# Optimization experiments

Measured on AMD Instinct MI355X. Metric: run time of the kernel, lower is better.

Reference implementation:

```python
import jax, jax.numpy as jnp
import numpy as np

N = 1024      # num nodes
E = 16384     # num edges
P = 8192      # num query pairs
HD1 = 64      # hidden_dim_1
HD2 = 64      # hidden_dim_2
VOCAB = 1000  # max_x + 1
EPS = 1e-5


def gcn_conv(x, W, b, src, dst, n):
    # PyG GCNConv: h = D^{-1/2} (A + I) D^{-1/2} (x @ W) + b
    h = x @ W
    loop = jnp.arange(n)
    s = jnp.concatenate([src, loop])
    d = jnp.concatenate([dst, loop])
    deg = jnp.zeros((n,), h.dtype).at[d].add(1.0)
    dis = jax.lax.rsqrt(deg)  # deg >= 1 due to self-loops
    norm = dis[s] * dis[d]
    out = jnp.zeros_like(h).at[d].add(norm[:, None] * h[s])
    return out + b


def graph_norm(x, w, b, alpha):
    # PyG GraphNorm with a single graph: stats over node dim (axis 0)
    mean = jnp.mean(x, axis=0, keepdims=True)
    sh = x - alpha * mean
    var = jnp.mean(sh * sh, axis=0, keepdims=True)
    return w * sh / jnp.sqrt(var + EPS) + b


def _forward(x_ids, ei, pos, emb, gW0, gb0, gnw0, gnb0, gna0, gW1, gb1,
             gnw1, gnb1, gna1, m1W, m1b, m2W, m2b, m3W, m3b,
             gn3w, gn3b, gn3a, ldW, ldb):
    n = x_ids.shape[0]
    src, dst = ei[0], ei[1]
    x = emb[x_ids]                                            # [n, HD1]
    # 1-WL: two GCNConv -> GraphNorm -> ReLU blocks
    x = jax.nn.relu(graph_norm(gcn_conv(x, gW0, gb0, src, dst, n), gnw0, gnb0, gna0))
    x = jax.nn.relu(graph_norm(gcn_conv(x, gW1, gb1, src, dst, n), gnw1, gnb1, gna1))
    # O(n^2) outer product: X[i,j] = x[i] * x[j]
    X = x[:, None, :] * x[None, :, :]                         # [n, n, HD1]
    eim = jnp.zeros((n, n), x.dtype).at[src, dst].set(1.0)    # adjacency indicator
    # add_chan = eye(n) @ eim = eim
    X = jnp.concatenate([X, eim[:, :, None]], axis=-1)        # [n, n, HD1+1]
    # 2-FWL refinement (layer2 = 1)
    x1 = jax.nn.relu(X @ m1W + m1b)                           # [n, n, HD2]
    x2 = jax.nn.relu(X @ m2W + m2b)                           # [n, n, HD2]
    prod = jnp.einsum('ikc,kjc->ijc', x1, x2)                 # per-channel bmm
    X = jnp.concatenate([X, prod], axis=-1)                   # [n, n, HD1+1+HD2]
    X = jax.nn.relu(graph_norm(X @ m3W + m3b, gn3w, gn3b, gn3a))
    # symmetric mul-pool then gather query pairs
    X = X * jnp.transpose(X, (1, 0, 2))                       # [n, n, HD2]
    feat = X[pos[:, 0], pos[:, 1]]                            # [P, HD2]
    return feat @ ldW + ldb                                   # [P, 1]


def setup_inputs() -> dict:
    key = jax.random.key(0)
    ks = jax.random.split(key, 12)
    sc = lambda k, s: jax.random.normal(k, s, jnp.float32) * 0.05
    d = {}
    d['x_ids'] = jax.random.randint(ks[0], (N,), 0, VOCAB)
    d['ei'] = jax.random.randint(ks[1], (2, E), 0, N)
    d['pos'] = jax.random.randint(ks[2], (P, 2), 0, N)
    d['emb'] = sc(ks[3], (VOCAB, HD1))
    d['gW0'] = sc(ks[4], (HD1, HD1)); d['gb0'] = jnp.zeros((HD1,), jnp.float32)
    d['gnw0'] = jnp.ones((HD1,), jnp.float32); d['gnb0'] = jnp.zeros((HD1,), jnp.float32); d['gna0'] = jnp.ones((HD1,), jnp.float32)
    d['gW1'] = sc(ks[5], (HD1, HD1)); d['gb1'] = jnp.zeros((HD1,), jnp.float32)
    d['gnw1'] = jnp.ones((HD1,), jnp.float32); d['gnb1'] = jnp.zeros((HD1,), jnp.float32); d['gna1'] = jnp.ones((HD1,), jnp.float32)
    d['m1W'] = sc(ks[6], (HD1 + 1, HD2)); d['m1b'] = jnp.zeros((HD2,), jnp.float32)
    d['m2W'] = sc(ks[7], (HD1 + 1, HD2)); d['m2b'] = jnp.zeros((HD2,), jnp.float32)
    d['m3W'] = sc(ks[8], (HD2 + HD1 + 1, HD2)); d['m3b'] = jnp.zeros((HD2,), jnp.float32)
    d['gn3w'] = jnp.ones((HD2,), jnp.float32); d['gn3b'] = jnp.zeros((HD2,), jnp.float32); d['gn3a'] = jnp.ones((HD2,), jnp.float32)
    d['ldW'] = sc(ks[9], (HD2, 1)); d['ldb'] = jnp.zeros((1,), jnp.float32)
    return d


def reference(x_ids, ei, pos, emb, gW0, gb0, gnw0, gnb0, gna0, gW1, gb1,
              gnw1, gnb1, gna1, m1W, m1b, m2W, m2b, m3W, m3b,
              gn3w, gn3b, gn3a, ldW, ldb):
    return _forward(x_ids, ei, pos, emb, gW0, gb0, gnw0, gnb0, gna0, gW1, gb1,
                    gnw1, gnb1, gna1, m1W, m1b, m2W, m2b, m3W, m3b,
                    gn3w, gn3b, gn3a, ldW, ldb)
```

## Files before the change

### kernel.cpp

```cpp
#include <hip/hip_runtime.h>


typedef unsigned short u16;
typedef unsigned int u32;

#define DI static __device__ __forceinline__

DI float bf2f(u16 u) { union { u32 i; float f; } v; v.i = ((u32)u) << 16; return v.f; }
DI u16 f2bf(float f) {
  union { float f; u32 i; } v; v.f = f;
  u32 u = v.i;
  return (u16)((u + 0x7fffu + ((u >> 16) & 1u)) >> 16);
}

typedef __bf16 bf16x8 __attribute__((ext_vector_type(8)));
typedef float f32x4 __attribute__((ext_vector_type(4)));

#define MFMA16(a, b, c) __builtin_amdgcn_mfma_f32_16x16x32_bf16((a), (b), (c), 0, 0, 0)

typedef const __attribute__((address_space(1))) u32* gas1;
typedef __attribute__((address_space(3))) u32* las3;


__global__ void k_setup(const int* __restrict__ xids, const float* __restrict__ emb,
                        float* __restrict__ xf, float* __restrict__ deg,
                        u32* __restrict__ eimu) {
  int g = blockIdx.x * 256 + threadIdx.x;
  if (g < 262144) eimu[g] = 0u;
  if (g < 1024) deg[g] = 1.0f;
  if (g < 65536) {
    int i = g >> 6, d = g & 63;
    xf[g] = emb[xids[i] * 64 + d];
  }
}

__global__ void k_edges(const int* __restrict__ ei, float* __restrict__ deg,
                        unsigned char* __restrict__ eim) {
  int e = blockIdx.x * 256 + threadIdx.x;
  if (e < 16384) {
    int s = ei[e], d = ei[16384 + e];
    atomicAdd(&deg[d], 1.0f);
    eim[s * 1024 + d] = 1;
  }
}

__global__ void k_gemm_node(const float* __restrict__ xf, const float* __restrict__ W,
                            const float* __restrict__ gb, const float* __restrict__ deg,
                            float* __restrict__ h, float* __restrict__ agg) {
  __shared__ float xrow[64];
  int i = blockIdx.x, c = threadIdx.x;
  xrow[c] = xf[i * 64 + c];
  __syncthreads();
  float s = 0.f;
#pragma unroll
  for (int d = 0; d < 64; ++d) s += xrow[d] * W[d * 64 + c];
  h[i * 64 + c] = s;
  agg[i * 64 + c] = s / deg[i] + gb[c];
}

__global__ void k_agg(const int* __restrict__ ei, const float* __restrict__ deg,
                      const float* __restrict__ h, float* __restrict__ agg) {
  int g = blockIdx.x * 256 + threadIdx.x;
  int e = g >> 6, c = g & 63;
  int s = ei[e], d = ei[16384 + e];
  float nrm = rsqrtf(deg[s]) * rsqrtf(deg[d]);
  atomicAdd(&agg[d * 64 + c], nrm * h[s * 64 + c]);
}

__global__ void k_gnorm(const float* __restrict__ agg, const float* __restrict__ gw,
                        const float* __restrict__ gbb, const float* __restrict__ ga,
                        float* __restrict__ xf, u16* __restrict__ xb, int last) {
  int c = blockIdx.x, t = threadIdx.x;
  float s = 0.f, ss = 0.f;
  for (int i = t; i < 1024; i += 256) {
    float v = agg[i * 64 + c];
    s += v; ss += v * v;
  }
  __shared__ float Ls[256], Lss[256];
  Ls[t] = s; Lss[t] = ss;
  __syncthreads();
  for (int off = 128; off > 0; off >>= 1) {
    if (t < off) { Ls[t] += Ls[t + off]; Lss[t] += Lss[t + off]; }
    __syncthreads();
  }
  float m = Ls[0] * (1.f / 1024.f);
  float a = ga[c];
  float var = Lss[0] * (1.f / 1024.f) - (2.f * a - a * a) * m * m;
  float sc = gw[c] * rsqrtf(fmaxf(var, 0.f) + 1e-5f);
  float bb = gbb[c];
  for (int i = t; i < 1024; i += 256) {
    float v = agg[i * 64 + c];
    float y = fmaxf(sc * (v - a * m) + bb, 0.f);
    xf[i * 64 + c] = y;
    if (last) xb[i * 64 + c] = f2bf(y);
  }
}

__global__ __launch_bounds__(256, 2) void k_build12(
    const u16* __restrict__ xbg, const unsigned char* __restrict__ eim,
    const float* __restrict__ m1W, const float* __restrict__ m1b,
    const float* __restrict__ m2W, const float* __restrict__ m2b,
    u16* __restrict__ x1tg, u16* __restrict__ x2tg, int cbase) {
  __shared__ u16 As[128 * 80];
  __shared__ u16 Bs[128 * 80];
  __shared__ u16 Cs[64 * 140];
  __shared__ unsigned char El[128 * 132];
  __shared__ float wsc[64];
  int b = blockIdx.x;
  int cg = b & 3;
  int rest = b >> 2;
  int which = rest >> 6;
  int t6 = rest & 63;
  int rbase = (t6 >> 3) * 128, sbase = (t6 & 7) * 128;
  const float* W = which ? m2W : m1W;
  const float* bias = which ? m2b : m1b;
  u16* outg = which ? x2tg : x1tg;
  int t = threadIdx.x;
  {
    int row = t >> 1, half = t & 1;
    const u32* gB = (const u32*)(xbg + (sbase + row) * 64 + half * 32);
    u32* dstB = (u32*)&Bs[row * 80 + half * 32];
#pragma unroll
    for (int k = 0; k < 16; ++k) dstB[k] = gB[k];
    int ab = which ? sbase : rbase;
    int bb = which ? rbase : sbase;
    const u32* gE = (const u32*)(eim + (size_t)(ab + row) * 1024 + bb + half * 64);
    u32* dstE = (u32*)&El[row * 132 + half * 64];
#pragma unroll
    for (int k = 0; k < 16; ++k) dstE[k] = gE[k];
  }
  int lane = t & 63, w = t >> 6;
  int q = lane >> 4, r = lane & 15;
  int wr = w >> 1, wc = w & 1;
  for (int ci = 0; ci < 4; ++ci) {
    int cl = cg * 4 + ci;
    int c = cbase + cl;
    if (t < 64) wsc[t] = W[t * 64 + c];
    __syncthreads();
    {
      int row = t >> 1, half = t & 1;
      const u32* ga = (const u32*)(xbg + (rbase + row) * 64 + half * 32);
      u32* dstA = (u32*)&As[row * 80 + half * 32];
#pragma unroll
      for (int k = 0; k < 16; ++k) {
        u32 u = ga[k];
        float f0 = bf2f((u16)(u & 0xffffu)) * wsc[half * 32 + 2 * k];
        float f1 = bf2f((u16)(u >> 16)) * wsc[half * 32 + 2 * k + 1];
        dstA[k] = (u32)f2bf(f0) | ((u32)f2bf(f1) << 16);
      }
    }
    __syncthreads();
    f32x4 z4 = {0.f, 0.f, 0.f, 0.f};
    f32x4 acc[4][4];
#pragma unroll
    for (int mi = 0; mi < 4; ++mi)
#pragma unroll
      for (int ni = 0; ni < 4; ++ni) acc[mi][ni] = z4;
#pragma unroll
    for (int ks = 0; ks < 2; ++ks) {
      bf16x8 af[4], bfr[4];
#pragma unroll
      for (int mi = 0; mi < 4; ++mi)
        af[mi] = *(const bf16x8*)&As[(wr * 64 + mi * 16 + r) * 80 + ks * 32 + q * 8];
#pragma unroll
      for (int ni = 0; ni < 4; ++ni)
        bfr[ni] = *(const bf16x8*)&Bs[(wc * 64 + ni * 16 + r) * 80 + ks * 32 + q * 8];
#pragma unroll
      for (int mi = 0; mi < 4; ++mi)
#pragma unroll
        for (int ni = 0; ni < 4; ++ni) acc[mi][ni] = MFMA16(af[mi], bfr[ni], acc[mi][ni]);
    }
    float w64 = W[64 * 64 + c];
    float bsv = bias[c];
#pragma unroll
    for (int mi = 0; mi < 4; ++mi) {
#pragma unroll
      for (int ni = 0; ni < 4; ++ni) {
        int col = wc * 64 + ni * 16 + r;
#pragma unroll
        for (int tt = 0; tt < 4; ++tt) {
          int row2 = wr * 64 + mi * 16 + q * 4 + tt;
          float e = (float)(which ? El[col * 132 + row2] : El[row2 * 132 + col]);
          acc[mi][ni][tt] = fmaxf(acc[mi][ni][tt] + e * w64 + bsv, 0.f);
        }
      }
    }
    u16* outp = outg + (size_t)cl * 1048576;
#pragma unroll
    for (int p = 0; p < 2; ++p) {
      __syncthreads();
      if (wr == p) {
#pragma unroll
        for (int mi = 0; mi < 4; ++mi)
#pragma unroll
          for (int ni = 0; ni < 4; ++ni) {
            int col = wc * 64 + ni * 16 + r;
#pragma unroll
            for (int tt = 0; tt < 4; ++tt) {
              int lrow = mi * 16 + q * 4 + tt;
              Cs[lrow * 140 + col] = f2bf(acc[mi][ni][tt]);
            }
          }
      }
      __syncthreads();
      {
        int rl = t >> 4, ch = t & 15;
#pragma unroll
        for (int it = 0; it < 4; ++it) {
          int row = it * 16 + rl;
          uint4 v = *(const uint4*)&Cs[row * 140 + ch * 8];
          *(uint4*)(outp + (size_t)(rbase + p * 64 + row) * 1024 + sbase + ch * 8) = v;
        }
      }
    }
  }
}

__global__ __launch_bounds__(256, 4) void k_prodgemm(
    const u16* __restrict__ x1tg, const u16* __restrict__ x2tg,
    u16* __restrict__ prod, int cbase) {
  __shared__ u16 pool[17408];
  int b = blockIdx.x;
  int cl = (b & 7) + ((b >> 9) << 3);
  int tile = (b >> 3) & 63;
  int i0 = (tile >> 3) * 128, j0 = (tile & 7) * 128;
  const u16* Ap = x1tg + (size_t)cl * 1048576;
  const u16* Bp = x2tg + (size_t)cl * 1048576;
  u16* Pp = prod + (size_t)(cbase + cl) * 1048576;
  int t = threadIdx.x, lane = t & 63, w = t >> 6;
  int q = lane >> 4, r = lane & 15;
  int wr = w >> 1, wc = w & 1;
  int srow = lane >> 2, scol = (lane & 3) * 8;

#define PSTAGE(KT)                                                          \
  {                                                                         \
    int pb_ = (KT) & 1;                                                     \
    int kk_ = (KT) * 32;                                                    \
    _Pragma("unroll")                                                       \
    for (int s = 0; s < 2; ++s) {                                           \
      int rowb = w * 32 + s * 16;                                           \
      __builtin_amdgcn_global_load_lds(                                     \
          (gas1)(Ap + (size_t)(i0 + rowb + srow) * 1024 + kk_ + scol),      \
          (las3)(pool + pb_ * 8192 + rowb * 32), 16, 0, 0);                 \
      __builtin_amdgcn_global_load_lds(                                     \
          (gas1)(Bp + (size_t)(j0 + rowb + srow) * 1024 + kk_ + scol),      \
          (las3)(pool + pb_ * 8192 + 4096 + rowb * 32), 16, 0, 0);          \
    }                                                                       \
  }

  f32x4 z4 = {0.f, 0.f, 0.f, 0.f};
  f32x4 acc[4][4];
#pragma unroll
  for (int mi = 0; mi < 4; ++mi)
#pragma unroll
    for (int ni = 0; ni < 4; ++ni) acc[mi][ni] = z4;

  PSTAGE(0);
#pragma unroll 2
  for (int kt = 0; kt < 32; ++kt) {
    int pb = kt & 1;
    if (kt < 31) {
      PSTAGE(kt + 1);
      asm volatile("s_waitcnt vmcnt(4)" ::: "memory");
    } else {
      asm volatile("s_waitcnt vmcnt(0)" ::: "memory");
    }
    __builtin_amdgcn_s_barrier();
    asm volatile("" ::: "memory");
    {
      bf16x8 af[4], bfr[4];
#pragma unroll
      for (int mi = 0; mi < 4; ++mi)
        af[mi] = *(const bf16x8*)&pool[pb * 8192 + (wr * 64 + mi * 16 + r) * 32 + q * 8];
#pragma unroll
      for (int ni = 0; ni < 4; ++ni)
        bfr[ni] = *(const bf16x8*)&pool[pb * 8192 + 4096 + (wc * 64 + ni * 16 + r) * 32 + q * 8];
#pragma unroll
      for (int mi = 0; mi < 4; ++mi)
#pragma unroll
        for (int ni = 0; ni < 4; ++ni) acc[mi][ni] = MFMA16(af[mi], bfr[ni], acc[mi][ni]);
    }
    asm volatile("s_waitcnt lgkmcnt(0)" ::: "memory");
    __builtin_amdgcn_s_barrier();
    asm volatile("" ::: "memory");
  }
#undef PSTAGE

  __syncthreads();
#pragma unroll
  for (int mi = 0; mi < 4; ++mi)
#pragma unroll
    for (int ni = 0; ni < 4; ++ni) {
      int col = wc * 64 + ni * 16 + r;
#pragma unroll
      for (int tt = 0; tt < 4; ++tt) {
        int row2 = wr * 64 + mi * 16 + q * 4 + tt;
        pool[row2 * 136 + col] = f2bf(acc[mi][ni][tt]);
      }
    }
  __syncthreads();
  {
    int rseg = t >> 4, cseg = t & 15;
#pragma unroll
    for (int it = 0; it < 8; ++it) {
      int row = it * 16 + rseg;
      uint4 v = *(const uint4*)&pool[row * 136 + cseg * 8];
      *(uint4*)(Pp + (size_t)(i0 + row) * 1024 + j0 + cseg * 8) = v;
    }
  }
}

__global__ __launch_bounds__(256, 3) void k_buildT(
    const u16* __restrict__ xbg, const unsigned char* __restrict__ eim,
    u16* PT, const float* __restrict__ m3W, const float* __restrict__ m3b,
    float* __restrict__ S, float* __restrict__ SS) {
  __shared__ __align__(16) u16 A[64 * 136];
  __shared__ u16 Wt[64 * 136];
  __shared__ u16 scratch[64 * 66];
  __shared__ __align__(16) u16 stg[64 * 72];
  __shared__ unsigned char eimrow[1024];
  int bx = blockIdx.x;
  int i = bx >> 1, bj = bx & 1;
  int jbase = bj * 512;
  int t = threadIdx.x, lane = t & 63, w = t >> 6;
  int q = lane >> 4, r = lane & 15;
  {
    int zidx = i * 256 + t;
    if (zidx < 65536) { S[zidx] = 0.f; SS[zidx] = 0.f; }
  }
  ((u32*)eimrow)[t] = ((const u32*)(eim + (size_t)i * 1024))[t];
  {
    int row = t >> 1, half = t & 1;
    int rsrc = row < 64 ? row : row + 1;
    float xsc = (row < 64) ? bf2f(xbg[i * 64 + row]) : 1.f;
    const float4* gw = (const float4*)(m3W + rsrc * 64 + half * 32);
#pragma unroll
    for (int k = 0; k < 8; ++k) {
      float4 f = gw[k];
      Wt[(half * 32 + 4 * k + 0) * 136 + row] = f2bf(f.x * xsc);
      Wt[(half * 32 + 4 * k + 1) * 136 + row] = f2bf(f.y * xsc);
      Wt[(half * 32 + 4 * k + 2) * 136 + row] = f2bf(f.z * xsc);
      Wt[(half * 32 + 4 * k + 3) * 136 + row] = f2bf(f.w * xsc);
    }
  }
  float w64c[4], b3c[4];
#pragma unroll
  for (int ni = 0; ni < 4; ++ni) {
    int cc = ni * 16 + r;
    w64c[ni] = m3W[64 * 64 + cc];
    b3c[ni] = m3b[cc];
  }
  int p4 = t >> 2, q4 = t & 3;
  uint4 pva, pvb, xva, xvb;
  {
    const uint4* gp = (const uint4*)(PT + (size_t)p4 * 1048576 + (size_t)i * 1024 + jbase + q4 * 16);
    pva = gp[0]; pvb = gp[1];
    const uint4* gx = (const uint4*)(xbg + (jbase + p4) * 64 + q4 * 16);
    xva = gx[0]; xvb = gx[1];
  }
  for (int jc8 = 0; jc8 < 8; ++jc8) {
    int j0 = jbase + jc8 * 64;
    asm volatile("s_waitcnt lgkmcnt(0)" ::: "memory");
    __builtin_amdgcn_s_barrier();
    asm volatile("" ::: "memory");
    {
      u32* sw = (u32*)&scratch[p4 * 66 + q4 * 16];
      sw[0] = pva.x; sw[1] = pva.y; sw[2] = pva.z; sw[3] = pva.w;
      sw[4] = pvb.x; sw[5] = pvb.y; sw[6] = pvb.z; sw[7] = pvb.w;
      *(uint4*)&A[p4 * 136 + q4 * 16] = xva;
      *(uint4*)&A[p4 * 136 + q4 * 16 + 8] = xvb;
    }
    if (jc8 < 7) {
      const uint4* gp = (const uint4*)(PT + (size_t)p4 * 1048576 + (size_t)i * 1024 + (j0 + 64) + q4 * 16);
      pva = gp[0]; pvb = gp[1];
      const uint4* gx = (const uint4*)(xbg + (j0 + 64 + p4) * 64 + q4 * 16);
      xva = gx[0]; xvb = gx[1];
    }
    if (jc8 > 0) {
      int pl = t >> 3, off = (t & 7) * 8;
#pragma unroll
      for (int k = 0; k < 2; ++k) {
        int plane = k * 32 + pl;
        uint4 v = *(const uint4*)&stg[plane * 72 + off];
        *(uint4*)(PT + (size_t)plane * 1048576 + (size_t)i * 1024 + (j0 - 64) + off) = v;
      }
    }
    asm volatile("s_waitcnt lgkmcnt(0)" ::: "memory");
    __builtin_amdgcn_s_barrier();
    asm volatile("" ::: "memory");
#pragma unroll
    for (int jj2 = 0; jj2 < 8; ++jj2) {
      int jr = w * 16 + jj2 * 2;
      u32 two = *(const u32*)&scratch[lane * 66 + jr];
      A[jr * 136 + 64 + lane] = (u16)(two & 0xffffu);
      A[(jr + 1) * 136 + 64 + lane] = (u16)(two >> 16);
    }
    asm volatile("s_waitcnt lgkmcnt(0)" ::: "memory");
    __builtin_amdgcn_s_barrier();
    asm volatile("" ::: "memory");
    f32x4 z4 = {0.f, 0.f, 0.f, 0.f};
    f32x4 acc[4];
#pragma unroll
    for (int ni = 0; ni < 4; ++ni) acc[ni] = z4;
#pragma unroll
    for (int ks = 0; ks < 4; ++ks) {
      bf16x8 af, bfr[4];
      af = *(const bf16x8*)&A[(w * 16 + r) * 136 + ks * 32 + q * 8];
#pragma unroll
      for (int ni = 0; ni < 4; ++ni)
        bfr[ni] = *(const bf16x8*)&Wt[(ni * 16 + r) * 136 + ks * 32 + q * 8];
#pragma unroll
      for (int ni = 0; ni < 4; ++ni) acc[ni] = MFMA16(af, bfr[ni], acc[ni]);
    }
#pragma unroll
    for (int tt = 0; tt < 4; ++tt) {
      int jj = w * 16 + q * 4 + tt;
      float ev = (float)eimrow[j0 + jj];
#pragma unroll
      for (int ni = 0; ni < 4; ++ni)
        acc[ni][tt] = acc[ni][tt] + ev * w64c[ni] + b3c[ni];
    }
#pragma unroll
    for (int ni = 0; ni < 4; ++ni) {
      int cc = ni * 16 + r;
      u32 lo = (u32)f2bf(acc[ni][0]) | ((u32)f2bf(acc[ni][1]) << 16);
      u32 hi = (u32)f2bf(acc[ni][2]) | ((u32)f2bf(acc[ni][3]) << 16);
      uint2 vv; vv.x = lo; vv.y = hi;
      *(uint2*)&stg[cc * 72 + w * 16 + q * 4] = vv;
    }
  }
  asm volatile("s_waitcnt lgkmcnt(0)" ::: "memory");
  __builtin_amdgcn_s_barrier();
  asm volatile("" ::: "memory");
  {
    int pl = t >> 3, off = (t & 7) * 8;
#pragma unroll
    for (int k = 0; k < 2; ++k) {
      int plane = k * 32 + pl;
      uint4 v = *(const uint4*)&stg[plane * 72 + off];
      *(uint4*)(PT + (size_t)plane * 1048576 + (size_t)i * 1024 + (jbase + 448) + off) = v;
    }
  }
}

__global__ void k_stats(const u16* __restrict__ Tg, float* __restrict__ S,
                        float* __restrict__ SS) {
  int b = blockIdx.x;
  int c = b >> 3, ic = b & 7;
  int t = threadIdx.x;
  const u16* base = Tg + (size_t)c * 1048576 + (size_t)ic * 131072 + t * 4;
  float s0 = 0.f, s1 = 0.f, s2 = 0.f, s3 = 0.f;
  float q0 = 0.f, q1 = 0.f, q2 = 0.f, q3 = 0.f;
  for (int ii = 0; ii < 128; ++ii) {
    uint2 u = *(const uint2*)(base + (size_t)ii * 1024);
    float v0 = bf2f((u16)(u.x & 0xffffu)), v1 = bf2f((u16)(u.x >> 16));
    float v2 = bf2f((u16)(u.y & 0xffffu)), v3 = bf2f((u16)(u.y >> 16));
    s0 += v0; q0 += v0 * v0;
    s1 += v1; q1 += v1 * v1;
    s2 += v2; q2 += v2 * v2;
    s3 += v3; q3 += v3 * v3;
  }
  int base2 = c * 1024 + t * 4;
  atomicAdd(&S[base2 + 0], s0);
  atomicAdd(&S[base2 + 1], s1);
  atomicAdd(&S[base2 + 2], s2);
  atomicAdd(&S[base2 + 3], s3);
  atomicAdd(&SS[base2 + 0], q0);
  atomicAdd(&SS[base2 + 1], q1);
  atomicAdd(&SS[base2 + 2], q2);
  atomicAdd(&SS[base2 + 3], q3);
}

__global__ void k_statsfin(const float* __restrict__ S, const float* __restrict__ SS,
                           const float* __restrict__ gn3w, const float* __restrict__ gn3b,
                           const float* __restrict__ gn3a,
                           float* __restrict__ normA, float* __restrict__ normB) {
  int idx = blockIdx.x * 256 + threadIdx.x;
  int c = idx & 63, j = idx >> 6;
  float sum = S[c * 1024 + j];
  float ssum = SS[c * 1024 + j];
  float m = sum * (1.f / 1024.f);
  float a = gn3a[c];
  float var = ssum * (1.f / 1024.f) - (2.f * a - a * a) * m * m;
  float sc = gn3w[c] * rsqrtf(fmaxf(var, 0.f) + 1e-5f);
  normA[idx] = sc;
  normB[idx] = gn3b[c] - sc * a * m;
}

__global__ void k_final(const u16* __restrict__ Tg, const float* __restrict__ normA,
                        const float* __restrict__ normB, const int* __restrict__ pos,
                        const float* __restrict__ ldW, const float* __restrict__ ldb,
                        float* __restrict__ out) {
  int t = threadIdx.x, w = t >> 6, lane = t & 63;
  int p = blockIdx.x * 4 + w;
  int i = pos[2 * p], j = pos[2 * p + 1];
  float t1 = bf2f(Tg[(size_t)lane * 1048576 + (size_t)i * 1024 + j]);
  float y1 = fmaxf(normA[j * 64 + lane] * t1 + normB[j * 64 + lane], 0.f);
  float t2 = bf2f(Tg[(size_t)lane * 1048576 + (size_t)j * 1024 + i]);
  float y2 = fmaxf(normA[i * 64 + lane] * t2 + normB[i * 64 + lane], 0.f);
  float z = y1 * y2 * ldW[lane];
#pragma unroll
  for (int off = 32; off > 0; off >>= 1) z += __shfl_down(z, off, 64);
  if (lane == 0) out[p] = z + ldb[0];
}

extern "C" void kernel_launch(void* const* d_in, const int* in_sizes, int n_in,
                              void* d_out, int out_size, void* d_ws, size_t ws_size,
                              hipStream_t stream) {
  const int* xids   = (const int*)d_in[0];
  const int* ei     = (const int*)d_in[1];
  const int* pos    = (const int*)d_in[2];
  const float* emb  = (const float*)d_in[3];
  const float* gW0  = (const float*)d_in[4];
  const float* gb0  = (const float*)d_in[5];
  const float* gnw0 = (const float*)d_in[6];
  const float* gnb0 = (const float*)d_in[7];
  const float* gna0 = (const float*)d_in[8];
  const float* gW1  = (const float*)d_in[9];
  const float* gb1  = (const float*)d_in[10];
  const float* gnw1 = (const float*)d_in[11];
  const float* gnb1 = (const float*)d_in[12];
  const float* gna1 = (const float*)d_in[13];
  const float* m1W  = (const float*)d_in[14];
  const float* m1b  = (const float*)d_in[15];
  const float* m2W  = (const float*)d_in[16];
  const float* m2b  = (const float*)d_in[17];
  const float* m3W  = (const float*)d_in[18];
  const float* m3b  = (const float*)d_in[19];
  const float* gn3w = (const float*)d_in[20];
  const float* gn3b = (const float*)d_in[21];
  const float* gn3a = (const float*)d_in[22];
  const float* ldW  = (const float*)d_in[23];
  const float* ldb  = (const float*)d_in[24];

  char* ws = (char*)d_ws;
  float* xf   = (float*)(ws + 0);
  float* h    = (float*)(ws + 262144);
  float* agg  = (float*)(ws + 524288);
  float* deg  = (float*)(ws + 786432);
  u16*   xb   = (u16*)(ws + 790528);
  unsigned char* eim = (unsigned char*)(ws + 921600);
  float* normA = (float*)(ws + 1970176);
  float* normB = (float*)(ws + 2232320);
  u16* x1tg = (u16*)(ws + 2494464);
  u16* x2tg = (u16*)(ws + 36048896);
  u16* prod = (u16*)(ws + 69603328);
  float* Sp  = (float*)x1tg;
  float* SSp = Sp + 65536;
  float* out = (float*)d_out;

  k_setup<<<1024, 256, 0, stream>>>(xids, emb, xf, deg, (u32*)eim);
  k_edges<<<64, 256, 0, stream>>>(ei, deg, eim);
  k_gemm_node<<<1024, 64, 0, stream>>>(xf, gW0, gb0, deg, h, agg);
  k_agg<<<4096, 256, 0, stream>>>(ei, deg, h, agg);
  k_gnorm<<<64, 256, 0, stream>>>(agg, gnw0, gnb0, gna0, xf, xb, 0);
  k_gemm_node<<<1024, 64, 0, stream>>>(xf, gW1, gb1, deg, h, agg);
  k_agg<<<4096, 256, 0, stream>>>(ei, deg, h, agg);
  k_gnorm<<<64, 256, 0, stream>>>(agg, gnw1, gnb1, gna1, xf, xb, 1);
  for (int g = 0; g < 4; ++g) {
    k_build12<<<512, 256, 0, stream>>>(xb, eim, m1W, m1b, m2W, m2b, x1tg, x2tg, g * 16);
    k_prodgemm<<<1024, 256, 0, stream>>>(x1tg, x2tg, prod, g * 16);
  }
  k_buildT<<<2048, 256, 0, stream>>>(xb, eim, prod, m3W, m3b, Sp, SSp);
  k_stats<<<512, 256, 0, stream>>>(prod, Sp, SSp);
  k_statsfin<<<256, 256, 0, stream>>>(Sp, SSp, gn3w, gn3b, gn3a, normA, normB);
  k_final<<<2048, 256, 0, stream>>>(prod, normA, normB, pos, ldW, ldb, out);
}
```

Measured before the change: 499.6 us.

## Restructure prodgemm to two waves with 64x128 warp tiles

The per-channel product GEMM block drops from four waves (each computing 64x64) to two waves, each computing a 64x128 sub-tile with 32 accumulators. Each wave issues more MFMAs per LDS fragment load, and the global-to-LDS staging is redistributed across the 128 threads. The epilogue now writes the tile back in two 64-row halves through a smaller LDS pool. In exchange, per-thread register use roughly doubles and each block has fewer waves to hide latency, which may cut occupancy.

Result: slower. 511.9 us (+2.5%).

```diff
diff --git a/kernel.cpp b/kernel.cpp
--- a/kernel.cpp
+++ b/kernel.cpp
@@ -216,10 +216,10 @@
   }
 }
 
-__global__ __launch_bounds__(256, 4) void k_prodgemm(
+__global__ __launch_bounds__(128, 2) void k_prodgemm(
     const u16* __restrict__ x1tg, const u16* __restrict__ x2tg,
     u16* __restrict__ prod, int cbase) {
-  __shared__ u16 pool[17408];
+  __shared__ u16 pool[16384];
   int b = blockIdx.x;
   int cl = (b & 7) + ((b >> 9) << 3);
   int tile = (b >> 3) & 63;
@@ -229,31 +229,30 @@
   u16* Pp = prod + (size_t)(cbase + cl) * 1048576;
   int t = threadIdx.x, lane = t & 63, w = t >> 6;
   int q = lane >> 4, r = lane & 15;
-  int wr = w >> 1, wc = w & 1;
-  int srow = lane >> 2, scol = (lane & 3) * 8;
+  int srow = t >> 2, scol = (t & 3) * 8;
 
 #define PSTAGE(KT)                                                          \
   {                                                                         \
     int pb_ = (KT) & 1;                                                     \
     int kk_ = (KT) * 32;                                                    \
     _Pragma("unroll")                                                       \
-    for (int s = 0; s < 2; ++s) {                                           \
-      int rowb = w * 32 + s * 16;                                           \
+    for (int s = 0; s < 4; ++s) {                                           \
+      int row_ = s * 32 + srow;                                             \
       __builtin_amdgcn_global_load_lds(                                     \
-          (gas1)(Ap + (size_t)(i0 + rowb + srow) * 1024 + kk_ + scol),      \
-          (las3)(pool + pb_ * 8192 + rowb * 32), 16, 0, 0);                 \
+          (gas1)(Ap + (size_t)(i0 + row_) * 1024 + kk_ + scol),             \
+          (las3)(pool + pb_ * 8192 + row_ * 32 + scol), 16, 0, 0);          \
       __builtin_amdgcn_global_load_lds(                                     \
-          (gas1)(Bp + (size_t)(j0 + rowb + srow) * 1024 + kk_ + scol),      \
-          (las3)(pool + pb_ * 8192 + 4096 + rowb * 32), 16, 0, 0);          \
+          (gas1)(Bp + (size_t)(j0 + row_) * 1024 + kk_ + scol),             \
+          (las3)(pool + pb_ * 8192 + 4096 + row_ * 32 + scol), 16, 0, 0);   \
     }                                                                       \
   }
 
   f32x4 z4 = {0.f, 0.f, 0.f, 0.f};
-  f32x4 acc[4][4];
+  f32x4 acc[4][8];
 #pragma unroll
   for (int mi = 0; mi < 4; ++mi)
 #pragma unroll
-    for (int ni = 0; ni < 4; ++ni) acc[mi][ni] = z4;
+    for (int n = 0; n < 8; ++n) acc[mi][n] = z4;
 
   PSTAGE(0);
 #pragma unroll 2
@@ -261,24 +260,24 @@
     int pb = kt & 1;
     if (kt < 31) {
       PSTAGE(kt + 1);
-      asm volatile("s_waitcnt vmcnt(4)" ::: "memory");
+      asm volatile("s_waitcnt vmcnt(8)" ::: "memory");
     } else {
       asm volatile("s_waitcnt vmcnt(0)" ::: "memory");
     }
     __builtin_amdgcn_s_barrier();
     asm volatile("" ::: "memory");
     {
-      bf16x8 af[4], bfr[4];
+      bf16x8 af[4], bfr[8];
 #pragma unroll
       for (int mi = 0; mi < 4; ++mi)
-        af[mi] = *(const bf16x8*)&pool[pb * 8192 + (wr * 64 + mi * 16 + r) * 32 + q * 8];
-#pragma unroll
-      for (int ni = 0; ni < 4; ++ni)
-        bfr[ni] = *(const bf16x8*)&pool[pb * 8192 + 4096 + (wc * 64 + ni * 16 + r) * 32 + q * 8];
+        af[mi] = *(const bf16x8*)&pool[pb * 8192 + (w * 64 + mi * 16 + r) * 32 + q * 8];
+#pragma unroll
+      for (int n = 0; n < 8; ++n)
+        bfr[n] = *(const bf16x8*)&pool[pb * 8192 + 4096 + (n * 16 + r) * 32 + q * 8];
 #pragma unroll
       for (int mi = 0; mi < 4; ++mi)
 #pragma unroll
-        for (int ni = 0; ni < 4; ++ni) acc[mi][ni] = MFMA16(af[mi], bfr[ni], acc[mi][ni]);
+        for (int n = 0; n < 8; ++n) acc[mi][n] = MFMA16(af[mi], bfr[n], acc[mi][n]);
     }
     asm volatile("s_waitcnt lgkmcnt(0)" ::: "memory");
     __builtin_amdgcn_s_barrier();
@@ -286,26 +285,29 @@
   }
 #undef PSTAGE
 
-  __syncthreads();
-#pragma unroll
-  for (int mi = 0; mi < 4; ++mi)
-#pragma unroll
-    for (int ni = 0; ni < 4; ++ni) {
-      int col = wc * 64 + ni * 16 + r;
-#pragma unroll
-      for (int tt = 0; tt < 4; ++tt) {
-        int row2 = wr * 64 + mi * 16 + q * 4 + tt;
-        pool[row2 * 136 + col] = f2bf(acc[mi][ni][tt]);
+#pragma unroll 1
+  for (int p = 0; p < 2; ++p) {
+    __syncthreads();
+    if (w == p) {
+#pragma unroll
+      for (int mi = 0; mi < 4; ++mi)
+#pragma unroll
+        for (int n = 0; n < 8; ++n)
+#pragma unroll
+          for (int tt = 0; tt < 4; ++tt) {
+            int lr = mi * 16 + q * 4 + tt;
+            pool[lr * 136 + n * 16 + r] = f2bf(acc[mi][n][tt]);
+          }
+    }
+    __syncthreads();
+    {
+      int rseg = t >> 4, cseg = t & 15;
+#pragma unroll
+      for (int it = 0; it < 8; ++it) {
+        int row = it * 8 + rseg;
+        uint4 v = *(const uint4*)&pool[row * 136 + cseg * 8];
+        *(uint4*)(Pp + (size_t)(i0 + p * 64 + row) * 1024 + j0 + cseg * 8) = v;
       }
-    }
-  __syncthreads();
-  {
-    int rseg = t >> 4, cseg = t & 15;
-#pragma unroll
-    for (int it = 0; it < 8; ++it) {
-      int row = it * 16 + rseg;
-      uint4 v = *(const uint4*)&pool[row * 136 + cseg * 8];
-      *(uint4*)(Pp + (size_t)(i0 + row) * 1024 + j0 + cseg * 8) = v;
     }
   }
 }
@@ -559,7 +561,7 @@
   k_gnorm<<<64, 256, 0, stream>>>(agg, gnw1, gnb1, gna1, xf, xb, 1);
   for (int g = 0; g < 4; ++g) {
     k_build12<<<512, 256, 0, stream>>>(xb, eim, m1W, m1b, m2W, m2b, x1tg, x2tg, g * 16);
-    k_prodgemm<<<1024, 256, 0, stream>>>(x1tg, x2tg, prod, g * 16);
+    k_prodgemm<<<1024, 128, 0, stream>>>(x1tg, x2tg, prod, g * 16);
   }
   k_buildT<<<2048, 256, 0, stream>>>(xb, eim, prod, m3W, m3b, Sp, SSp);
   k_stats<<<512, 256, 0, stream>>>(prod, Sp, SSp);
```
